# Kernel tuning notes

Measured on AMD Instinct MI355X. Metric: run time of the kernel, lower is better.

## Reference

```python
import jax, jax.numpy as jnp
import numpy as np
import math

N_HEAD = 16
LATENT_RANK = 64

def setup_inputs() -> dict:
    key = jax.random.key(0)
    ks = jax.random.split(key, 8)
    B, T, C, H, R = 4, 2048, 1024, N_HEAD, LATENT_RANK
    std = 0.02
    return {
        "hidden_states": jax.random.normal(ks[0], (B, T, C), jnp.float32),
        "basis_w": jax.random.normal(ks[1], (R, C), jnp.float32) * std,
        "core": jax.random.normal(ks[2], (R, R), jnp.float32) * std,
        "head_residual": jax.random.normal(ks[3], (H, R, R), jnp.float32) * (std / 10.0),
        "v_w": jax.random.normal(ks[4], (C, C), jnp.float32) * std,
        "v_b": jnp.zeros((C,), jnp.float32),
        "o_w": jax.random.normal(ks[5], (C, C), jnp.float32) * std,
        "o_b": jnp.zeros((C,), jnp.float32),
    }

def reference(hidden_states, basis_w, core, head_residual, v_w, v_b, o_w, o_b):
    B, T, C = hidden_states.shape
    H = N_HEAD
    R = LATENT_RANK
    head_dim = C // H

    # latent projection: [B,T,R]
    latent = jnp.einsum('btc,rc->btr', hidden_states, basis_w)

    # symmetric core + centered per-head residual -> head matrices [H,R,R]
    core_sym = 0.5 * (core + core.T)
    centered = head_residual - head_residual.mean(axis=0, keepdims=True)
    head_mats = core_sym[None] / float(H) + centered

    # bilinear latent attention scores [B,H,T,T]
    lt = jnp.einsum('btr,hrs->bhts', latent, head_mats)  # fold Q-transform
    att = jnp.einsum('bhts,bus->bhtu', lt, latent) * (1.0 / math.sqrt(R))

    # causal mask + softmax
    causal = jnp.tril(jnp.ones((T, T), jnp.bool_))
    att = jnp.where(causal[None, None], att, jnp.float32(-jnp.inf))
    att = jax.nn.softmax(att, axis=-1)

    # value projection [B,H,T,head_dim]
    v = (hidden_states @ v_w.T + v_b).reshape(B, T, H, head_dim).transpose(0, 2, 1, 3)
    y = att @ v  # [B,H,T,head_dim]
    y = y.transpose(0, 2, 1, 3).reshape(B, T, C)
    y = y @ o_w.T + o_b
    return y
```

## Files before the change

### kernel.cpp

```cpp
#include <hip/hip_runtime.h>
#include <hip/hip_bf16.h>


#define N_HEAD 16
#define RANK 64

typedef __attribute__((ext_vector_type(8))) short bf16x8;
typedef __attribute__((ext_vector_type(4))) float f32x4;

__device__ __forceinline__ ushort f2b(float f) {
    unsigned u = __builtin_bit_cast(unsigned, f);
    u += 0x7fffu + ((u >> 16) & 1u);
    return (ushort)(u >> 16);
}

__device__ __forceinline__ int swz(int row, int col) {
    return (row << 6) | (col ^ ((row & 7) << 3));
}

__global__ void cvt_kernel(const float* __restrict__ src, ushort* __restrict__ dst, int n4) {
    int i = blockIdx.x * blockDim.x + threadIdx.x;
    if (i >= n4) return;
    float4 v = ((const float4*)src)[i];
    ushort4 o;
    o.x = f2b(v.x); o.y = f2b(v.y); o.z = f2b(v.z); o.w = f2b(v.w);
    ((ushort4*)dst)[i] = o;
}

__global__ void headmats_kernel(const float* __restrict__ core,
                                const float* __restrict__ resid,
                                ushort* __restrict__ hmT) {
    int idx = blockIdx.x * 256 + threadIdx.x;
    if (idx >= RANK * RANK) return;
    int r = idx >> 6, s = idx & 63;
    float mean = 0.f;
    for (int h = 0; h < N_HEAD; ++h) mean += resid[h * RANK * RANK + idx];
    mean *= (1.0f / N_HEAD);
    float cs = 0.5f * (core[r * RANK + s] + core[s * RANK + r]) * (1.0f / N_HEAD);
    for (int h = 0; h < N_HEAD; ++h) {
        float val = cs + resid[h * RANK * RANK + idx] - mean;
        hmT[h * RANK * RANK + s * RANK + r] = f2b(val);
    }
}

__global__ __launch_bounds__(256) void gemm_nt(
    const ushort* __restrict__ A, const ushort* __restrict__ W,
    const float* __restrict__ bias,
    float* __restrict__ outF, ushort* __restrict__ outB,
    int M, int N, int K,
    int zDivA, long long aStride, int zModW, long long wStride, long long oStride,
    int outVT)
{
    __shared__ ushort As[128 * 72];
    __shared__ ushort Ws[64 * 72];

    int z = blockIdx.z;
    A += (size_t)(z / zDivA) * aStride;
    W += (size_t)(z % zModW) * wStride;
    size_t obase = (size_t)z * oStride;

    int m0 = blockIdx.y * 128;
    int n0 = blockIdx.x * 64;
    int t = threadIdx.x;
    int wave = t >> 6, lane = t & 63;
    int wr = wave >> 1, wc = wave & 1;
    int g = lane >> 4, ln = lane & 15;

    f32x4 acc[4][2];
    for (int i = 0; i < 4; ++i)
        for (int j = 0; j < 2; ++j) acc[i][j] = (f32x4){0.f, 0.f, 0.f, 0.f};

    for (int k0 = 0; k0 < K; k0 += 64) {
        for (int q = 0; q < 4; ++q) {
            int e = (t + 256 * q) * 8;
            int row = e >> 6, col = e & 63;
            *(bf16x8*)&As[row * 72 + col] =
                *(const bf16x8*)(A + (size_t)(m0 + row) * K + k0 + col);
        }
        for (int q = 0; q < 2; ++q) {
            int e = (t + 256 * q) * 8;
            int row = e >> 6, col = e & 63;
            *(bf16x8*)&Ws[row * 72 + col] =
                *(const bf16x8*)(W + (size_t)(n0 + row) * K + k0 + col);
        }
        __syncthreads();
        for (int ks = 0; ks < 2; ++ks) {
            bf16x8 a[4], b[2];
            for (int fm = 0; fm < 4; ++fm)
                a[fm] = *(const bf16x8*)&As[(wr * 64 + fm * 16 + ln) * 72 + ks * 32 + 8 * g];
            for (int fn = 0; fn < 2; ++fn)
                b[fn] = *(const bf16x8*)&Ws[(wc * 32 + fn * 16 + ln) * 72 + ks * 32 + 8 * g];
            for (int fm = 0; fm < 4; ++fm)
                for (int fn = 0; fn < 2; ++fn)
                    acc[fm][fn] = __builtin_amdgcn_mfma_f32_16x16x32_bf16(
                        a[fm], b[fn], acc[fm][fn], 0, 0, 0);
        }
        __syncthreads();
    }

    if (outVT) {
        for (int fm = 0; fm < 4; ++fm)
            for (int fn = 0; fn < 2; ++fn) {
                int row = m0 + wr * 64 + fm * 16 + 4 * g;
                int col = n0 + wc * 32 + fn * 16 + ln;
                float bv = bias ? bias[col] : 0.f;
                ushort4 us;
                us.x = f2b(acc[fm][fn][0] + bv);
                us.y = f2b(acc[fm][fn][1] + bv);
                us.z = f2b(acc[fm][fn][2] + bv);
                us.w = f2b(acc[fm][fn][3] + bv);
                size_t off = ((size_t)(row >> 11) * 1024 + col) * 2048 + (row & 2047);
                *(ushort4*)(outB + off) = us;
            }
    } else {
        for (int fm = 0; fm < 4; ++fm)
            for (int fn = 0; fn < 2; ++fn)
                for (int r = 0; r < 4; ++r) {
                    int row = m0 + wr * 64 + fm * 16 + 4 * g + r;
                    int col = n0 + wc * 32 + fn * 16 + ln;
                    float val = acc[fm][fn][r];
                    if (bias) val += bias[col];
                    size_t o = obase + (size_t)row * N + col;
                    if (outF) outF[o] = val;
                    if (outB) outB[o] = f2b(val);
                }
    }
}

__global__ __launch_bounds__(256) void attn_kernel(
    const ushort* __restrict__ lt, const ushort* __restrict__ latent,
    const ushort* __restrict__ vT, ushort* __restrict__ y)
{
    const int T = 2048, C = 1024;
    __shared__ ushort Ps[4][32 * 64];

    int pq = blockIdx.x, h = blockIdx.y, b = blockIdx.z;
    int t = threadIdx.x, w = t >> 6, lane = t & 63;
    int g = lane >> 4, ln = lane & 15;

    const ushort* Kg = latent + (size_t)b * T * RANK;
    const ushort* Vg = vT + (size_t)(b * N_HEAD + h) * 64 * T;
    ushort* Pw = Ps[w];

    const float SCL = 0.125f * 1.44269504089f;
    const float THR = 11.5f;

    for (int pass = 0; pass < 2; ++pass) {
        int qt = pass ? (15 - pq) : pq;
        int qrow0 = qt * 128 + w * 32;

        const ushort* Qg = lt + ((size_t)(b * N_HEAD + h) * T + qrow0) * RANK;
        bf16x8 qa[2][2];
        for (int m = 0; m < 2; ++m)
            for (int ks = 0; ks < 2; ++ks)
                qa[m][ks] = *(const bf16x8*)(Qg + (size_t)(m * 16 + ln) * RANK + ks * 32 + 8 * g);

        float mr[2][4], lp[2][4];
        f32x4 o[2][4];
        for (int m = 0; m < 2; ++m)
            for (int r = 0; r < 4; ++r) { mr[m][r] = -INFINITY; lp[m][r] = 0.f; }
        for (int m = 0; m < 2; ++m)
            for (int fn = 0; fn < 4; ++fn) o[m][fn] = (f32x4){0.f, 0.f, 0.f, 0.f};

        int kmax = 2 * qt + 1;
        for (int kt = 0; kt <= kmax; ++kt) {
            f32x4 s[2][4];
            for (int m = 0; m < 2; ++m)
                for (int fn = 0; fn < 4; ++fn) s[m][fn] = (f32x4){0.f, 0.f, 0.f, 0.f};
            for (int ks = 0; ks < 2; ++ks) {
                bf16x8 kb[4];
                for (int fn = 0; fn < 4; ++fn)
                    kb[fn] = *(const bf16x8*)(Kg +
                        (size_t)(kt * 64 + fn * 16 + ln) * RANK + ks * 32 + 8 * g);
                for (int m = 0; m < 2; ++m)
                    for (int fn = 0; fn < 4; ++fn)
                        s[m][fn] = __builtin_amdgcn_mfma_f32_16x16x32_bf16(
                            qa[m][ks], kb[fn], s[m][fn], 0, 0, 0);
            }

            bf16x8 vb[2][4];
            for (int ks = 0; ks < 2; ++ks)
                for (int fn = 0; fn < 4; ++fn)
                    vb[ks][fn] = *(const bf16x8*)(Vg +
                        (size_t)(fn * 16 + ln) * T + kt * 64 + ks * 32 + 8 * g);

            float rm[2][4];
            for (int m = 0; m < 2; ++m) {
                for (int r = 0; r < 4; ++r) rm[m][r] = -INFINITY;
                int qb = qrow0 + m * 16 + 4 * g;
                if ((kt * 64 + 63) > (qrow0 + m * 16)) {
                    for (int fn = 0; fn < 4; ++fn) {
                        int key = kt * 64 + fn * 16 + ln;
                        for (int r = 0; r < 4; ++r) {
                            float sv = s[m][fn][r] * SCL;
                            if (key > qb + r) sv = -INFINITY;
                            s[m][fn][r] = sv;
                            rm[m][r] = fmaxf(rm[m][r], sv);
                        }
                    }
                } else {
                    for (int fn = 0; fn < 4; ++fn)
                        for (int r = 0; r < 4; ++r) {
                            float sv = s[m][fn][r] * SCL;
                            s[m][fn][r] = sv;
                            rm[m][r] = fmaxf(rm[m][r], sv);
                        }
                }
            }

            int need = 0;
            for (int m = 0; m < 2; ++m)
                for (int r = 0; r < 4; ++r) need |= (rm[m][r] > mr[m][r] + THR);
            if (__any(need)) {
                for (int off = 1; off < 16; off <<= 1)
                    for (int m = 0; m < 2; ++m)
                        for (int r = 0; r < 4; ++r)
                            rm[m][r] = fmaxf(rm[m][r], __shfl_xor(rm[m][r], off));
                for (int m = 0; m < 2; ++m)
                    for (int r = 0; r < 4; ++r) {
                        float nm = fmaxf(mr[m][r], rm[m][r]);
                        float al = exp2f(mr[m][r] - nm);
                        mr[m][r] = nm;
                        lp[m][r] *= al;
                        for (int fn = 0; fn < 4; ++fn) o[m][fn][r] *= al;
                    }
            }

            for (int m = 0; m < 2; ++m)
                for (int fn = 0; fn < 4; ++fn)
                    for (int r = 0; r < 4; ++r) {
                        float p = exp2f(s[m][fn][r] - mr[m][r]);
                        lp[m][r] += p;
                        Pw[swz(m * 16 + 4 * g + r, fn * 16 + ln)] = f2b(p);
                    }

            for (int ks = 0; ks < 2; ++ks) {
                bf16x8 pa[2];
                for (int m = 0; m < 2; ++m)
                    pa[m] = *(const bf16x8*)&Pw[swz(m * 16 + ln, ks * 32 + 8 * g)];
                for (int m = 0; m < 2; ++m)
                    for (int fn = 0; fn < 4; ++fn)
                        o[m][fn] = __builtin_amdgcn_mfma_f32_16x16x32_bf16(
                            pa[m], vb[ks][fn], o[m][fn], 0, 0, 0);
            }
        }

        for (int off = 1; off < 16; off <<= 1)
            for (int m = 0; m < 2; ++m)
                for (int r = 0; r < 4; ++r) lp[m][r] += __shfl_xor(lp[m][r], off);
        for (int m = 0; m < 2; ++m)
            for (int fn = 0; fn < 4; ++fn)
                for (int r = 0; r < 4; ++r) {
                    int row = qrow0 + m * 16 + 4 * g + r;
                    y[((size_t)b * T + row) * C + h * 64 + fn * 16 + ln] =
                        f2b(o[m][fn][r] / lp[m][r]);
                }
    }
}

extern "C" void kernel_launch(void* const* d_in, const int* in_sizes, int n_in,
                              void* d_out, int out_size, void* d_ws, size_t ws_size,
                              hipStream_t stream) {
    const float* hs    = (const float*)d_in[0];
    const float* basis = (const float*)d_in[1];
    const float* core  = (const float*)d_in[2];
    const float* resid = (const float*)d_in[3];
    const float* v_w   = (const float*)d_in[4];
    const float* v_b   = (const float*)d_in[5];
    const float* o_w   = (const float*)d_in[6];
    const float* o_b   = (const float*)d_in[7];
    float* out = (float*)d_out;

    const int B = 4, T = 2048, C = 1024, H = N_HEAD, R = RANK;
    const int M = B * T;

    char* ws = (char*)d_ws;
    ushort* hs_b    = (ushort*)(ws + 0);
    ushort* y_b     = hs_b;
    ushort* basis_b = (ushort*)(ws + 16777216);
    ushort* vw_b    = (ushort*)(ws + 16908288);
    ushort* ow_b    = (ushort*)(ws + 19005440);
    ushort* hm_b    = (ushort*)(ws + 21102592);
    ushort* lat_b   = (ushort*)(ws + 21233664);
    ushort* lt_b    = (ushort*)(ws + 22282240);
    ushort* vT_b    = (ushort*)(ws + 39059456);

    cvt_kernel<<<dim3(M * C / 4 / 256), 256, 0, stream>>>(hs, hs_b, M * C / 4);
    cvt_kernel<<<dim3(R * C / 4 / 256), 256, 0, stream>>>(basis, basis_b, R * C / 4);
    cvt_kernel<<<dim3(C * C / 4 / 256), 256, 0, stream>>>(v_w, vw_b, C * C / 4);
    cvt_kernel<<<dim3(C * C / 4 / 256), 256, 0, stream>>>(o_w, ow_b, C * C / 4);

    headmats_kernel<<<dim3(16), 256, 0, stream>>>(core, resid, hm_b);

    gemm_nt<<<dim3(1, M / 128, 1), 256, 0, stream>>>(
        hs_b, basis_b, nullptr, nullptr, lat_b, M, R, C, 1, 0, 1, 0, 0, 0);

    gemm_nt<<<dim3(C / 64, M / 128, 1), 256, 0, stream>>>(
        hs_b, vw_b, v_b, nullptr, vT_b, M, C, C, 1, 0, 1, 0, 0, 1);

    gemm_nt<<<dim3(1, T / 128, B * H), 256, 0, stream>>>(
        lat_b, hm_b, nullptr, nullptr, lt_b, T, R, R,
        H, (long long)T * R, H, (long long)R * R, (long long)T * R, 0);

    attn_kernel<<<dim3(8, H, B), 256, 0, stream>>>(lt_b, lat_b, vT_b, y_b);

    gemm_nt<<<dim3(C / 64, M / 128, 1), 256, 0, stream>>>(
        y_b, ow_b, o_b, out, nullptr, M, C, C, 1, 0, 1, 0, 0, 0);
}
```

Measured before the change: 340.5 us.

## Split attention KV loop across wave pairs, fold softmax scale, widen GEMM tiles

The attention kernel goes to 512 threads, with two waves per 32-row query slab. Each wave handles alternating key tiles, and the two partial softmax states are merged through shared memory at the end. The softmax scale is folded into the head matrices, P is converted to bf16 by truncation instead of rounding, and V loads are moved next to their MFMAs. The large GEMMs use a 128-wide N tile through a template parameter. These changes aim to add parallelism and latency hiding in attention and reuse in the GEMMs, at the cost of extra shared memory, barriers, register pressure and slightly lower precision.

```diff
diff --git a/kernel.cpp b/kernel.cpp
--- a/kernel.cpp
+++ b/kernel.cpp
@@ -12,6 +12,10 @@
     unsigned u = __builtin_bit_cast(unsigned, f);
     u += 0x7fffu + ((u >> 16) & 1u);
     return (ushort)(u >> 16);
+}
+
+__device__ __forceinline__ ushort f2b_trunc(float f) {
+    return (ushort)(__builtin_bit_cast(unsigned, f) >> 16);
 }
 
 __device__ __forceinline__ int swz(int row, int col) {
@@ -30,6 +34,7 @@
 __global__ void headmats_kernel(const float* __restrict__ core,
                                 const float* __restrict__ resid,
                                 ushort* __restrict__ hmT) {
+    const float SCLF = 0.125f * 1.44269504089f;
     int idx = blockIdx.x * 256 + threadIdx.x;
     if (idx >= RANK * RANK) return;
     int r = idx >> 6, s = idx & 63;
@@ -38,11 +43,12 @@
     mean *= (1.0f / N_HEAD);
     float cs = 0.5f * (core[r * RANK + s] + core[s * RANK + r]) * (1.0f / N_HEAD);
     for (int h = 0; h < N_HEAD; ++h) {
-        float val = cs + resid[h * RANK * RANK + idx] - mean;
+        float val = (cs + resid[h * RANK * RANK + idx] - mean) * SCLF;
         hmT[h * RANK * RANK + s * RANK + r] = f2b(val);
     }
 }
 
+template<int BN>
 __global__ __launch_bounds__(256) void gemm_nt(
     const ushort* __restrict__ A, const ushort* __restrict__ W,
     const float* __restrict__ bias,
@@ -51,8 +57,9 @@
     int zDivA, long long aStride, int zModW, long long wStride, long long oStride,
     int outVT)
 {
+    constexpr int FN = BN / 32;
     __shared__ ushort As[128 * 72];
-    __shared__ ushort Ws[64 * 72];
+    __shared__ ushort Ws[BN * 72];
 
     int z = blockIdx.z;
     A += (size_t)(z / zDivA) * aStride;
@@ -60,15 +67,15 @@
     size_t obase = (size_t)z * oStride;
 
     int m0 = blockIdx.y * 128;
-    int n0 = blockIdx.x * 64;
+    int n0 = blockIdx.x * BN;
     int t = threadIdx.x;
     int wave = t >> 6, lane = t & 63;
     int wr = wave >> 1, wc = wave & 1;
     int g = lane >> 4, ln = lane & 15;
 
-    f32x4 acc[4][2];
+    f32x4 acc[4][FN];
     for (int i = 0; i < 4; ++i)
-        for (int j = 0; j < 2; ++j) acc[i][j] = (f32x4){0.f, 0.f, 0.f, 0.f};
+        for (int j = 0; j < FN; ++j) acc[i][j] = (f32x4){0.f, 0.f, 0.f, 0.f};
 
     for (int k0 = 0; k0 < K; k0 += 64) {
         for (int q = 0; q < 4; ++q) {
@@ -77,7 +84,7 @@
             *(bf16x8*)&As[row * 72 + col] =
                 *(const bf16x8*)(A + (size_t)(m0 + row) * K + k0 + col);
         }
-        for (int q = 0; q < 2; ++q) {
+        for (int q = 0; q < BN / 32; ++q) {
             int e = (t + 256 * q) * 8;
             int row = e >> 6, col = e & 63;
             *(bf16x8*)&Ws[row * 72 + col] =
@@ -85,13 +92,13 @@
         }
         __syncthreads();
         for (int ks = 0; ks < 2; ++ks) {
-            bf16x8 a[4], b[2];
+            bf16x8 a[4], b[FN];
             for (int fm = 0; fm < 4; ++fm)
                 a[fm] = *(const bf16x8*)&As[(wr * 64 + fm * 16 + ln) * 72 + ks * 32 + 8 * g];
-            for (int fn = 0; fn < 2; ++fn)
-                b[fn] = *(const bf16x8*)&Ws[(wc * 32 + fn * 16 + ln) * 72 + ks * 32 + 8 * g];
+            for (int fn = 0; fn < FN; ++fn)
+                b[fn] = *(const bf16x8*)&Ws[(wc * (BN / 2) + fn * 16 + ln) * 72 + ks * 32 + 8 * g];
             for (int fm = 0; fm < 4; ++fm)
-                for (int fn = 0; fn < 2; ++fn)
+                for (int fn = 0; fn < FN; ++fn)
                     acc[fm][fn] = __builtin_amdgcn_mfma_f32_16x16x32_bf16(
                         a[fm], b[fn], acc[fm][fn], 0, 0, 0);
         }
@@ -100,9 +107,9 @@
 
     if (outVT) {
         for (int fm = 0; fm < 4; ++fm)
-            for (int fn = 0; fn < 2; ++fn) {
+            for (int fn = 0; fn < FN; ++fn) {
                 int row = m0 + wr * 64 + fm * 16 + 4 * g;
-                int col = n0 + wc * 32 + fn * 16 + ln;
+                int col = n0 + wc * (BN / 2) + fn * 16 + ln;
                 float bv = bias ? bias[col] : 0.f;
                 ushort4 us;
                 us.x = f2b(acc[fm][fn][0] + bv);
@@ -114,10 +121,10 @@
             }
     } else {
         for (int fm = 0; fm < 4; ++fm)
-            for (int fn = 0; fn < 2; ++fn)
+            for (int fn = 0; fn < FN; ++fn)
                 for (int r = 0; r < 4; ++r) {
                     int row = m0 + wr * 64 + fm * 16 + 4 * g + r;
-                    int col = n0 + wc * 32 + fn * 16 + ln;
+                    int col = n0 + wc * (BN / 2) + fn * 16 + ln;
                     float val = acc[fm][fn][r];
                     if (bias) val += bias[col];
                     size_t o = obase + (size_t)row * N + col;
@@ -127,27 +134,28 @@
     }
 }
 
-__global__ __launch_bounds__(256) void attn_kernel(
+__global__ __launch_bounds__(512, 4) void attn_kernel(
     const ushort* __restrict__ lt, const ushort* __restrict__ latent,
     const ushort* __restrict__ vT, ushort* __restrict__ y)
 {
     const int T = 2048, C = 1024;
-    __shared__ ushort Ps[4][32 * 64];
+    __shared__ ushort Ps[8][32 * 64];
+    __shared__ float Oex[4][64][36];
+    __shared__ float Mex[4][32], Lex[4][32];
 
     int pq = blockIdx.x, h = blockIdx.y, b = blockIdx.z;
     int t = threadIdx.x, w = t >> 6, lane = t & 63;
     int g = lane >> 4, ln = lane & 15;
+    int hf = w >> 1, par = w & 1;
 
     const ushort* Kg = latent + (size_t)b * T * RANK;
     const ushort* Vg = vT + (size_t)(b * N_HEAD + h) * 64 * T;
     ushort* Pw = Ps[w];
-
-    const float SCL = 0.125f * 1.44269504089f;
     const float THR = 11.5f;
 
     for (int pass = 0; pass < 2; ++pass) {
         int qt = pass ? (15 - pq) : pq;
-        int qrow0 = qt * 128 + w * 32;
+        int qrow0 = qt * 128 + hf * 32;
 
         const ushort* Qg = lt + ((size_t)(b * N_HEAD + h) * T + qrow0) * RANK;
         bf16x8 qa[2][2];
@@ -162,8 +170,8 @@
         for (int m = 0; m < 2; ++m)
             for (int fn = 0; fn < 4; ++fn) o[m][fn] = (f32x4){0.f, 0.f, 0.f, 0.f};
 
-        int kmax = 2 * qt + 1;
-        for (int kt = 0; kt <= kmax; ++kt) {
+        int kmax = 2 * qt + (hf >> 1);
+        for (int kt = par; kt <= kmax; kt += 2) {
             f32x4 s[2][4];
             for (int m = 0; m < 2; ++m)
                 for (int fn = 0; fn < 4; ++fn) s[m][fn] = (f32x4){0.f, 0.f, 0.f, 0.f};
@@ -178,21 +186,15 @@
                             qa[m][ks], kb[fn], s[m][fn], 0, 0, 0);
             }
 
-            bf16x8 vb[2][4];
-            for (int ks = 0; ks < 2; ++ks)
-                for (int fn = 0; fn < 4; ++fn)
-                    vb[ks][fn] = *(const bf16x8*)(Vg +
-                        (size_t)(fn * 16 + ln) * T + kt * 64 + ks * 32 + 8 * g);
-
             float rm[2][4];
             for (int m = 0; m < 2; ++m) {
                 for (int r = 0; r < 4; ++r) rm[m][r] = -INFINITY;
                 int qb = qrow0 + m * 16 + 4 * g;
-                if ((kt * 64 + 63) > (qrow0 + m * 16)) {
+                if (kt * 64 + 63 > qrow0 + m * 16) {
                     for (int fn = 0; fn < 4; ++fn) {
                         int key = kt * 64 + fn * 16 + ln;
                         for (int r = 0; r < 4; ++r) {
-                            float sv = s[m][fn][r] * SCL;
+                            float sv = s[m][fn][r];
                             if (key > qb + r) sv = -INFINITY;
                             s[m][fn][r] = sv;
                             rm[m][r] = fmaxf(rm[m][r], sv);
@@ -200,11 +202,8 @@
                     }
                 } else {
                     for (int fn = 0; fn < 4; ++fn)
-                        for (int r = 0; r < 4; ++r) {
-                            float sv = s[m][fn][r] * SCL;
-                            s[m][fn][r] = sv;
-                            rm[m][r] = fmaxf(rm[m][r], sv);
-                        }
+                        for (int r = 0; r < 4; ++r)
+                            rm[m][r] = fmaxf(rm[m][r], s[m][fn][r]);
                 }
             }
 
@@ -231,30 +230,62 @@
                     for (int r = 0; r < 4; ++r) {
                         float p = exp2f(s[m][fn][r] - mr[m][r]);
                         lp[m][r] += p;
-                        Pw[swz(m * 16 + 4 * g + r, fn * 16 + ln)] = f2b(p);
+                        Pw[swz(m * 16 + 4 * g + r, fn * 16 + ln)] = f2b_trunc(p);
                     }
 
             for (int ks = 0; ks < 2; ++ks) {
                 bf16x8 pa[2];
                 for (int m = 0; m < 2; ++m)
                     pa[m] = *(const bf16x8*)&Pw[swz(m * 16 + ln, ks * 32 + 8 * g)];
+                for (int fn = 0; fn < 4; ++fn) {
+                    bf16x8 vb = *(const bf16x8*)(Vg +
+                        (size_t)(fn * 16 + ln) * T + kt * 64 + ks * 32 + 8 * g);
+                    for (int m = 0; m < 2; ++m)
+                        o[m][fn] = __builtin_amdgcn_mfma_f32_16x16x32_bf16(
+                            pa[m], vb, o[m][fn], 0, 0, 0);
+                }
+            }
+        }
+
+        for (int off = 1; off < 16; off <<= 1)
+            for (int m = 0; m < 2; ++m)
+                for (int r = 0; r < 4; ++r) lp[m][r] += __shfl_xor(lp[m][r], off);
+
+        if (par) {
+            for (int m = 0; m < 2; ++m)
+                for (int fn = 0; fn < 4; ++fn)
+                    *(f32x4*)&Oex[hf][fn * 16 + ln][m * 16 + 4 * g] = o[m][fn];
+            if (ln == 0)
                 for (int m = 0; m < 2; ++m)
-                    for (int fn = 0; fn < 4; ++fn)
-                        o[m][fn] = __builtin_amdgcn_mfma_f32_16x16x32_bf16(
-                            pa[m], vb[ks][fn], o[m][fn], 0, 0, 0);
-            }
-        }
-
-        for (int off = 1; off < 16; off <<= 1)
-            for (int m = 0; m < 2; ++m)
-                for (int r = 0; r < 4; ++r) lp[m][r] += __shfl_xor(lp[m][r], off);
-        for (int m = 0; m < 2; ++m)
-            for (int fn = 0; fn < 4; ++fn)
+                    for (int r = 0; r < 4; ++r) {
+                        Mex[hf][m * 16 + 4 * g + r] = mr[m][r];
+                        Lex[hf][m * 16 + 4 * g + r] = lp[m][r];
+                    }
+        }
+        __syncthreads();
+
+        if (!par) {
+            for (int m = 0; m < 2; ++m) {
+                float a0[4], sc1[4], li[4];
                 for (int r = 0; r < 4; ++r) {
-                    int row = qrow0 + m * 16 + 4 * g + r;
-                    y[((size_t)b * T + row) * C + h * 64 + fn * 16 + ln] =
-                        f2b(o[m][fn][r] / lp[m][r]);
-                }
+                    int row = m * 16 + 4 * g + r;
+                    float mo = Mex[hf][row], lo = Lex[hf][row];
+                    float Mx = fmaxf(mr[m][r], mo);
+                    a0[r] = exp2f(mr[m][r] - Mx);
+                    sc1[r] = exp2f(mo - Mx);
+                    li[r] = 1.0f / (lp[m][r] * a0[r] + lo * sc1[r]);
+                }
+                for (int fn = 0; fn < 4; ++fn) {
+                    f32x4 Oo = *(const f32x4*)&Oex[hf][fn * 16 + ln][m * 16 + 4 * g];
+                    for (int r = 0; r < 4; ++r) {
+                        int row = qrow0 + m * 16 + 4 * g + r;
+                        float val = (o[m][fn][r] * a0[r] + Oo[r] * sc1[r]) * li[r];
+                        y[((size_t)b * T + row) * C + h * 64 + fn * 16 + ln] = f2b(val);
+                    }
+                }
+            }
+        }
+        __syncthreads();
     }
 }
 
@@ -292,18 +323,18 @@
 
     headmats_kernel<<<dim3(16), 256, 0, stream>>>(core, resid, hm_b);
 
-    gemm_nt<<<dim3(1, M / 128, 1), 256, 0, stream>>>(
+    gemm_nt<64><<<dim3(1, M / 128, 1), 256, 0, stream>>>(
         hs_b, basis_b, nullptr, nullptr, lat_b, M, R, C, 1, 0, 1, 0, 0, 0);
 
-    gemm_nt<<<dim3(C / 64, M / 128, 1), 256, 0, stream>>>(
+    gemm_nt<128><<<dim3(C / 128, M / 128, 1), 256, 0, stream>>>(
         hs_b, vw_b, v_b, nullptr, vT_b, M, C, C, 1, 0, 1, 0, 0, 1);
 
-    gemm_nt<<<dim3(1, T / 128, B * H), 256, 0, stream>>>(
+    gemm_nt<64><<<dim3(1, T / 128, B * H), 256, 0, stream>>>(
         lat_b, hm_b, nullptr, nullptr, lt_b, T, R, R,
         H, (long long)T * R, H, (long long)R * R, (long long)T * R, 0);
 
-    attn_kernel<<<dim3(8, H, B), 256, 0, stream>>>(lt_b, lat_b, vT_b, y_b);
-
-    gemm_nt<<<dim3(C / 64, M / 128, 1), 256, 0, stream>>>(
+    attn_kernel<<<dim3(8, H, B), 512, 0, stream>>>(lt_b, lat_b, vT_b, y_b);
+
+    gemm_nt<128><<<dim3(C / 128, M / 128, 1), 256, 0, stream>>>(
         y_b, ow_b, o_b, out, nullptr, M, C, C, 1, 0, 1, 0, 0, 0);
 }
```

After: 488.2 us. +43.4%, slower.
